# Kernel optimization log

Hardware: AMD Instinct MI355X
Metric: run time of the kernel (lower is better)

Reference implementation:

```python
import jax, jax.numpy as jnp
import numpy as np

D, P, S, E = 200, 200, 150, 150  # drugs, proteins, diseases, side-effects
EMB = 256

def setup_inputs() -> dict:
    key = jax.random.key(0)
    ks = jax.random.split(key, 10)
    s = 0.05
    type_mask = jnp.concatenate([
        jnp.zeros(D, jnp.int64) if False else jnp.full((D,), 0, jnp.int32),
        jnp.full((P,), 1, jnp.int32),
        jnp.full((S,), 2, jnp.int32),
        jnp.full((E,), 3, jnp.int32)]).astype(jnp.int32)
    return {
        'type_mask': type_mask,
        'entity_embedding': jax.random.normal(ks[0], (D + P + S + E, EMB)) * s,
        'relation_embedding': jax.random.normal(ks[1], (1200, EMB)) * s,
        'W_ent': jax.random.normal(ks[2], (EMB, EMB)) * s,
        'W_rel': jax.random.normal(ks[3], (EMB, EMB)) * s,
        'W1': jax.random.normal(ks[4], (2 * EMB, 1024)) * s,
        'b1': jnp.zeros((1024,)),
        'W2': jax.random.normal(ks[5], (1024, 512)) * s,
        'b2': jnp.zeros((512,)),
        'W3': jax.random.normal(ks[6], (512, 2)) * s,
        'b3': jnp.zeros((2,)),
    }

def _pair_softmax(a, b, W1, b1, W2, b2, W3, b3):
    # classifier(concat(a[i], b[j])) for the full cartesian product.
    # First linear is decomposed: W1 @ [a;b] = a@W1a + b@W1b (same math,
    # avoids materializing the [Na*Nb, 2*EMB] concat tensor).
    W1a, W1b = W1[:EMB], W1[EMB:]
    ha = a @ W1a                      # [Na, 1024]
    hb = b @ W1b                      # [Nb, 1024]
    h = jax.nn.relu(ha[:, None, :] + hb[None, :, :] + b1)  # [Na, Nb, 1024]
    h = jax.nn.relu(h @ W2 + b2)      # [Na, Nb, 512]
    logits = h @ W3 + b3              # [Na, Nb, 2]
    Na, Nb = a.shape[0], b.shape[0]
    return jax.nn.softmax(logits.reshape(Na * Nb, 2), axis=-1)

def reference(type_mask, entity_embedding, relation_embedding, W_ent, W_rel,
              W1, b1, W2, b2, W3, b3):
    tm = np.asarray(type_mask)  # concrete, block-structured type ids
    idx = [np.nonzero(tm == t)[0] for t in range(4)]
    # project embeddings (project_on path; nn.Linear: x @ W)
    ent = entity_embedding @ W_ent
    _rel = relation_embedding @ W_rel  # computed in original forward, unused (graph_on off)
    drug, prot, dis, se = (ent[idx[0]], ent[idx[1]], ent[idx[2]], ent[idx[3]])
    cls = lambda a, b: _pair_softmax(a, b, W1, b1, W2, b2, W3, b3)
    out_dp = cls(drug, prot)
    out_dd = cls(drug, drug)
    out_ds = cls(drug, dis)
    out_de = cls(drug, se)
    out_ps = cls(prot, dis)
    out_pp = cls(prot, prot)
    out_pd = cls(prot, drug)
    out_ed = cls(se, drug)
    out_sp = cls(dis, prot)
    out_sd = cls(dis, drug)
    return (out_dp, out_dd, out_ds, out_de, out_ps, out_pp, out_pd,
            out_ed, out_sp, out_sd, drug)
```

## Files before the change

kernel.cpp:

```cpp
#include <hip/hip_runtime.h>
#include <hip/hip_bf16.h>

typedef __attribute__((ext_vector_type(4))) float floatx4;
typedef __attribute__((ext_vector_type(8))) __bf16 bf16x8;
typedef unsigned short ushort_t;

#define NENT  700
#define EMB   256
#define KDIM  1024
#define NDIM  512
#define HROWS 720
#define NPAIR 340000

#define WS_HA   0
#define WS_HB   (WS_HA + HROWS*KDIM*2)
#define WS_W2H  (WS_HB + HROWS*KDIM*2)
#define WS_ENT  (WS_W2H + NDIM*KDIM*2)
#define WS_LG   (WS_ENT + NENT*EMB*4)

__device__ __forceinline__ float ldin(const void* p, int i, int isbf) {
    return isbf ? __bfloat162float(((const __hip_bfloat16*)p)[i])
                : ((const float*)p)[i];
}

__device__ __forceinline__ int detect_bf16(const ushort_t* __restrict__ w) {
    int t = threadIdx.x & 63;
    int e = (w[2*t] >> 7) & 0xFF;
    unsigned long long m = __ballot(e >= 100 && e <= 126);
    return (__popcll(m) >= 48) ? 1 : 0;
}

#define LDS_BARRIER() do { __builtin_amdgcn_s_waitcnt(0xC07F); __builtin_amdgcn_s_barrier(); } while (0)

__global__ void entprep_kernel(const void* __restrict__ E, const void* __restrict__ Went,
                               const void* __restrict__ W2,
                               float* __restrict__ ent, __hip_bfloat16* __restrict__ W2H,
                               void* __restrict__ out) {
    int isbf = detect_bf16((const ushort_t*)E);
    if (blockIdx.x < 88) {
        int ib = blockIdx.x * 8, t = threadIdx.x;
        __shared__ float rows[8][EMB];
#pragma unroll
        for (int r = 0; r < 8; ++r) {
            int i = ib + r;
            rows[r][t] = (i < NENT) ? ldin(E, i*EMB + t, isbf) : 0.f;
        }
        __syncthreads();
        float acc[8] = {0.f,0.f,0.f,0.f,0.f,0.f,0.f,0.f};
        if (isbf) {
            const __hip_bfloat16* W = (const __hip_bfloat16*)Went;
            for (int k = 0; k < EMB; ++k) {
                float w = __bfloat162float(W[k*EMB + t]);
#pragma unroll
                for (int r = 0; r < 8; ++r) acc[r] += rows[r][k] * w;
            }
        } else {
            const float* W = (const float*)Went;
            for (int k = 0; k < EMB; ++k) {
                float w = W[k*EMB + t];
#pragma unroll
                for (int r = 0; r < 8; ++r) acc[r] += rows[r][k] * w;
            }
        }
#pragma unroll
        for (int r = 0; r < 8; ++r) {
            int i = ib + r;
            if (i < NENT) {
                ent[i*EMB + t] = acc[r];
                if (i < 200) {
                    if (isbf) ((__hip_bfloat16*)out)[680000 + i*EMB + t] = __float2bfloat16(acc[r]);
                    else      ((float*)out)[680000 + i*EMB + t] = acc[r];
                }
            }
        }
    } else {
        int g = (blockIdx.x - 88)*256 + threadIdx.x;
        int lane = g & 63, f = (g >> 6) & 15, kc = (g >> 10) & 31, half = g >> 15;
        int l15 = lane & 15, quad = lane >> 4;
        int n = half*256 + f*16 + l15;
        bf16x8 v;
#pragma unroll
        for (int j = 0; j < 8; ++j) {
            int k = kc*32 + quad*8 + j;
            v[j] = (__bf16)ldin(W2, k*NDIM + n, isbf);
        }
        *(bf16x8*)(W2H + (size_t)g*8) = v;
    }
}

__global__ void hab_kernel(const float* __restrict__ ent, const void* __restrict__ E,
                           const void* __restrict__ W1, const void* __restrict__ b1,
                           __hip_bfloat16* __restrict__ HA, __hip_bfloat16* __restrict__ HB) {
    int isbf = detect_bf16((const ushort_t*)E);
    int part = blockIdx.y;
    int ib = blockIdx.x * 16;
    int t = threadIdx.x;
    __shared__ float rows[16][EMB];
#pragma unroll
    for (int r = 0; r < 16; ++r) {
        int i = ib + r;
        rows[r][t] = (i < NENT) ? ent[i*EMB + t] : 0.f;
    }
    __syncthreads();
    float acc[16][4];
#pragma unroll
    for (int r = 0; r < 16; ++r)
#pragma unroll
        for (int p = 0; p < 4; ++p) acc[r][p] = 0.f;

    int wbase = part*EMB*KDIM;
    if (isbf) {
        const __hip_bfloat16* W = (const __hip_bfloat16*)W1;
        for (int k = 0; k < EMB; ++k) {
            float w[4];
#pragma unroll
            for (int p = 0; p < 4; ++p) w[p] = __bfloat162float(W[wbase + k*KDIM + t + p*256]);
#pragma unroll
            for (int r = 0; r < 16; ++r) {
                float e = rows[r][k];
#pragma unroll
                for (int p = 0; p < 4; ++p) acc[r][p] += e * w[p];
            }
        }
    } else {
        const float* W = (const float*)W1;
        for (int k = 0; k < EMB; ++k) {
            float w[4];
#pragma unroll
            for (int p = 0; p < 4; ++p) w[p] = W[wbase + k*KDIM + t + p*256];
#pragma unroll
            for (int r = 0; r < 16; ++r) {
                float e = rows[r][k];
#pragma unroll
                for (int p = 0; p < 4; ++p) acc[r][p] += e * w[p];
            }
        }
    }
    __hip_bfloat16* HX = part ? HB : HA;
#pragma unroll
    for (int r = 0; r < 16; ++r) {
#pragma unroll
        for (int p = 0; p < 4; ++p) {
            int n = t + p*256;
            float v = acc[r][p];
            if (!part) v += ldin(b1, n, isbf);
            HX[(ib + r)*KDIM + n] = __float2bfloat16(v);
        }
    }
}

union U8 { bf16x8 v; unsigned u[4]; };

__device__ __forceinline__ bf16x8 mk_af3(bf16x8 ha, bf16x8 hb) {
    U8 r;
#pragma unroll
    for (int j = 0; j < 4; ++j) {
        float x0 = fmaxf((float)ha[2*j]   + (float)hb[2*j],   0.f);
        float x1 = fmaxf((float)ha[2*j+1] + (float)hb[2*j+1], 0.f);
        unsigned u0 = __float_as_uint(x0) + 0x8000u;
        unsigned u1 = __float_as_uint(x1) + 0x8000u;
#if defined(__has_builtin) && __has_builtin(__builtin_amdgcn_perm)
        r.u[j] = __builtin_amdgcn_perm(u1, u0, 0x07060302u);
#else
        r.u[j] = (u0 >> 16) | (u1 & 0xFFFF0000u);
#endif
    }
    return r.v;
}

#define MFMA(a, b, c) __builtin_amdgcn_mfma_f32_16x16x32_bf16((a), (b), (c), 0, 0, 0)

__global__ __launch_bounds__(512, 2) void pair_kernel(
        const ushort_t* __restrict__ HA, const ushort_t* __restrict__ HB,
        const ushort_t* __restrict__ W2H, const void* __restrict__ E,
        const void* __restrict__ b2, const void* __restrict__ W3,
        const void* __restrict__ b3, void* __restrict__ out) {

    const int blkEnd[10] = {325,650,900,1150,1400,1725,2050,2297,2544,2791};
    const int aB[10]  = {0,0,0,0,200,200,200,550,400,400};
    const int bB[10]  = {200,0,400,550,400,200,0,0,200,0};
    const int NaT[10] = {200,200,200,200,200,200,200,150,150,150};
    const int NbT[10] = {200,200,150,150,150,200,200,200,200,200};
    const int jTl[10] = {13,13,10,10,10,13,13,13,13,13};
    const int oOf[10] = {0,80000,160000,220000,280000,340000,420000,500000,560000,620000};

    __shared__ __align__(16) unsigned char sAF[32768];
    __shared__ float lgt[8][128][2];

    int bid = blockIdx.x;
    int ty = 0;
    while (bid >= blkEnd[ty]) ty++;
    int lb = bid - (ty ? blkEnd[ty-1] : 0);
    int jT = jTl[ty];
    int it = lb / jT;
    int jt = lb - it*jT;
    int i0 = aB[ty] + it*8;
    int j0 = bB[ty] + jt*16;

    int tid  = threadIdx.x;
    int lane = tid & 63;
    int w    = tid >> 6;
    int kcw  = w & 1;
    int mp   = (w >> 1) * 2;
    int l15  = lane & 15;
    int quad = lane >> 4;
    int kb   = (bid*7) & 31;

    const char* WB = (const char*)W2H + ((size_t)((w>>2)*512 + (w&3)*4))*1024 + lane*16;
    const ushort_t* HBp  = HB + (j0 + l15)*KDIM + quad*8;
    const ushort_t* HAp0 = HA + (i0 + mp)*KDIM + quad*8;
    const ushort_t* HAp1 = HAp0 + KDIM;

    floatx4 acc[8][4];
#pragma unroll
    for (int mf = 0; mf < 8; ++mf)
#pragma unroll
        for (int nf = 0; nf < 4; ++nf) acc[mf][nf] = (floatx4){0.f,0.f,0.f,0.f};

    int k0 = kb, k1 = (kb + 1) & 31;
    bf16x8 Bc0 = *(const bf16x8*)(WB + (size_t)k0*16384);
    bf16x8 Bc1 = *(const bf16x8*)(WB + (size_t)k0*16384 + 1024);
    bf16x8 Bc2 = *(const bf16x8*)(WB + (size_t)k0*16384 + 2048);
    bf16x8 Bc3 = *(const bf16x8*)(WB + (size_t)k0*16384 + 3072);
    bf16x8 Bn0 = *(const bf16x8*)(WB + (size_t)k1*16384);
    bf16x8 Bn1 = *(const bf16x8*)(WB + (size_t)k1*16384 + 1024);
    bf16x8 Bn2 = *(const bf16x8*)(WB + (size_t)k1*16384 + 2048);
    bf16x8 Bn3 = *(const bf16x8*)(WB + (size_t)k1*16384 + 3072);

    int kg0 = (kb + kcw) & 31;
    bf16x8 ha0 = *(const bf16x8*)(HAp0 + kg0*32);
    bf16x8 ha1 = *(const bf16x8*)(HAp1 + kg0*32);
    bf16x8 hb  = *(const bf16x8*)(HBp + kg0*32);

#define MFMA4(mf, x, B0, B1, B2, B3)                         \
    acc[mf][0] = MFMA(x, B0, acc[mf][0]);                    \
    acc[mf][1] = MFMA(x, B1, acc[mf][1]);                    \
    acc[mf][2] = MFMA(x, B2, acc[mf][2]);                    \
    acc[mf][3] = MFMA(x, B3, acc[mf][3]);

#pragma unroll 2
    for (int ph = 0; ph < 16; ++ph) {
        char* sW = (char*)sAF + (ph & 1)*16384 + kcw*8192 + mp*1024 + lane*16;
        *(bf16x8*)(sW)        = mk_af3(ha0, hb);
        *(bf16x8*)(sW + 1024) = mk_af3(ha1, hb);
        int kgn = (kb + 2*(ph + 1) + kcw) & 31;
        ha0 = *(const bf16x8*)(HAp0 + kgn*32);
        ha1 = *(const bf16x8*)(HAp1 + kgn*32);
        hb  = *(const bf16x8*)(HBp + kgn*32);
        LDS_BARRIER();

        const char* sR = (const char*)sAF + (ph & 1)*16384 + lane*16;
        int kn2 = (kb + 2*ph + 2) & 31;
        int kn3 = (kb + 2*ph + 3) & 31;
        {
            bf16x8 x0 = *(const bf16x8*)(sR);
            bf16x8 x1 = *(const bf16x8*)(sR + 1024);
            bf16x8 x2 = *(const bf16x8*)(sR + 2048);
            MFMA4(0, x0, Bc0, Bc1, Bc2, Bc3); x0 = *(const bf16x8*)(sR + 3072);
            MFMA4(1, x1, Bc0, Bc1, Bc2, Bc3); x1 = *(const bf16x8*)(sR + 4096);
            MFMA4(2, x2, Bc0, Bc1, Bc2, Bc3); x2 = *(const bf16x8*)(sR + 5120);
            MFMA4(3, x0, Bc0, Bc1, Bc2, Bc3); x0 = *(const bf16x8*)(sR + 6144);
            MFMA4(4, x1, Bc0, Bc1, Bc2, Bc3); x1 = *(const bf16x8*)(sR + 7168);
            MFMA4(5, x2, Bc0, Bc1, Bc2, Bc3);
            MFMA4(6, x0, Bc0, Bc1, Bc2, Bc3);
            MFMA4(7, x1, Bc0, Bc1, Bc2, Bc3);
        }
        Bc0 = *(const bf16x8*)(WB + (size_t)kn2*16384);
        Bc1 = *(const bf16x8*)(WB + (size_t)kn2*16384 + 1024);
        Bc2 = *(const bf16x8*)(WB + (size_t)kn2*16384 + 2048);
        Bc3 = *(const bf16x8*)(WB + (size_t)kn2*16384 + 3072);
        {
            bf16x8 x0 = *(const bf16x8*)(sR + 8192);
            bf16x8 x1 = *(const bf16x8*)(sR + 8192 + 1024);
            bf16x8 x2 = *(const bf16x8*)(sR + 8192 + 2048);
            MFMA4(0, x0, Bn0, Bn1, Bn2, Bn3); x0 = *(const bf16x8*)(sR + 8192 + 3072);
            MFMA4(1, x1, Bn0, Bn1, Bn2, Bn3); x1 = *(const bf16x8*)(sR + 8192 + 4096);
            MFMA4(2, x2, Bn0, Bn1, Bn2, Bn3); x2 = *(const bf16x8*)(sR + 8192 + 5120);
            MFMA4(3, x0, Bn0, Bn1, Bn2, Bn3); x0 = *(const bf16x8*)(sR + 8192 + 6144);
            MFMA4(4, x1, Bn0, Bn1, Bn2, Bn3); x1 = *(const bf16x8*)(sR + 8192 + 7168);
            MFMA4(5, x2, Bn0, Bn1, Bn2, Bn3);
            MFMA4(6, x0, Bn0, Bn1, Bn2, Bn3);
            MFMA4(7, x1, Bn0, Bn1, Bn2, Bn3);
        }
        Bn0 = *(const bf16x8*)(WB + (size_t)kn3*16384);
        Bn1 = *(const bf16x8*)(WB + (size_t)kn3*16384 + 1024);
        Bn2 = *(const bf16x8*)(WB + (size_t)kn3*16384 + 2048);
        Bn3 = *(const bf16x8*)(WB + (size_t)kn3*16384 + 3072);
    }
#undef MFMA4

    int isbf = detect_bf16((const ushort_t*)E);
    int nb = w*64;
    float b2v[4], wa[4], wb[4];
#pragma unroll
    for (int nf = 0; nf < 4; ++nf) {
        int n = nb + nf*16 + l15;
        b2v[nf] = ldin(b2, n, isbf);
        wa[nf]  = ldin(W3, 2*n, isbf);
        wb[nf]  = ldin(W3, 2*n+1, isbf);
    }
#pragma unroll
    for (int mf = 0; mf < 8; ++mf) {
        float s0[4] = {0.f,0.f,0.f,0.f};
        float s1[4] = {0.f,0.f,0.f,0.f};
#pragma unroll
        for (int nf = 0; nf < 4; ++nf) {
            floatx4 c = acc[mf][nf];
#pragma unroll
            for (int r = 0; r < 4; ++r) {
                float v = fmaxf(c[r] + b2v[nf], 0.f);
                s0[r] += v * wa[nf];
                s1[r] += v * wb[nf];
            }
        }
#pragma unroll
        for (int off = 1; off < 16; off <<= 1) {
#pragma unroll
            for (int r = 0; r < 4; ++r) {
                s0[r] += __shfl_xor(s0[r], off, 64);
                s1[r] += __shfl_xor(s1[r], off, 64);
            }
        }
        if (l15 == 0) {
#pragma unroll
            for (int r = 0; r < 4; ++r) {
                int p = mf*16 + quad*4 + r;
                lgt[w][p][0] = s0[r];
                lgt[w][p][1] = s1[r];
            }
        }
    }
    __syncthreads();

    if (tid < 128) {
        int p = tid;
        float l0 = 0.f, l1 = 0.f;
#pragma unroll
        for (int ww = 0; ww < 8; ++ww) { l0 += lgt[ww][p][0]; l1 += lgt[ww][p][1]; }
        l0 += ldin(b3, 0, isbf);
        l1 += ldin(b3, 1, isbf);
        int pi = it*8 + (p >> 4), pj = jt*16 + (p & 15);
        if (pi < NaT[ty] && pj < NbT[ty]) {
            float mx = fmaxf(l0, l1);
            float e0 = __expf(l0 - mx), e1 = __expf(l1 - mx);
            float inv = 1.f / (e0 + e1);
            int o = oOf[ty] + (pi*NbT[ty] + pj)*2;
            if (isbf) {
                __hip_bfloat16* ob = (__hip_bfloat16*)out;
                ob[o]   = __float2bfloat16(e0 * inv);
                ob[o+1] = __float2bfloat16(e1 * inv);
            } else {
                float* of = (float*)out;
                of[o]   = e0 * inv;
                of[o+1] = e1 * inv;
            }
        }
    }
}

extern "C" void kernel_launch(void* const* d_in, const int* in_sizes, int n_in,
                              void* d_out, int out_size, void* d_ws, size_t ws_size,
                              hipStream_t stream) {
    const void* E    = d_in[1];
    const void* Went = d_in[3];
    const void* W1   = d_in[5];
    const void* b1   = d_in[6];
    const void* W2   = d_in[7];
    const void* b2   = d_in[8];
    const void* W3   = d_in[9];
    const void* b3   = d_in[10];

    char* ws = (char*)d_ws;
    __hip_bfloat16* HA   = (__hip_bfloat16*)(ws + WS_HA);
    __hip_bfloat16* HB   = (__hip_bfloat16*)(ws + WS_HB);
    __hip_bfloat16* W2H  = (__hip_bfloat16*)(ws + WS_W2H);
    float*          entf = (float*)(ws + WS_ENT);

    entprep_kernel<<<dim3(344), dim3(256), 0, stream>>>(E, Went, W2, entf, W2H, d_out);
    hab_kernel<<<dim3(45, 2), dim3(256), 0, stream>>>(entf, E, W1, b1, HA, HB);
    pair_kernel<<<dim3(2791), dim3(512), 0, stream>>>((const ushort_t*)HA, (const ushort_t*)HB,
                                                      (const ushort_t*)W2H, E, b2, W3, b3, d_out);
}
```

Baseline: 514.8 us.

## Halve pair tile rows and give each wave both N halves of W2

The pair kernel now uses 256-thread blocks covering 4 A-rows by 16 B-columns (64 pairs) instead of 8x16, with twice as many blocks. Each of the 4 waves now covers 128 output columns (two 64-column slices from each N half), holding 8 B fragments and a 4x8 accumulator tile. The aim is better load balance and occupancy with smaller blocks and less LDS. In exchange, W2 fragments are reused across fewer pair rows per block, so more W2 traffic from L2, and the main loop is no longer unrolled.

```diff
diff --git a/kernel.cpp b/kernel.cpp
--- a/kernel.cpp
+++ b/kernel.cpp
@@ -170,13 +170,13 @@
 
 #define MFMA(a, b, c) __builtin_amdgcn_mfma_f32_16x16x32_bf16((a), (b), (c), 0, 0, 0)
 
-__global__ __launch_bounds__(512, 2) void pair_kernel(
+__global__ __launch_bounds__(256, 2) void pair_kernel(
         const ushort_t* __restrict__ HA, const ushort_t* __restrict__ HB,
         const ushort_t* __restrict__ W2H, const void* __restrict__ E,
         const void* __restrict__ b2, const void* __restrict__ W3,
         const void* __restrict__ b3, void* __restrict__ out) {
 
-    const int blkEnd[10] = {325,650,900,1150,1400,1725,2050,2297,2544,2791};
+    const int blkEnd[10] = {650,1300,1800,2300,2800,3450,4100,4594,5088,5582};
     const int aB[10]  = {0,0,0,0,200,200,200,550,400,400};
     const int bB[10]  = {200,0,400,550,400,200,0,0,200,0};
     const int NaT[10] = {200,200,200,200,200,200,200,150,150,150};
@@ -184,8 +184,8 @@
     const int jTl[10] = {13,13,10,10,10,13,13,13,13,13};
     const int oOf[10] = {0,80000,160000,220000,280000,340000,420000,500000,560000,620000};
 
-    __shared__ __align__(16) unsigned char sAF[32768];
-    __shared__ float lgt[8][128][2];
+    __shared__ __align__(16) unsigned char sAF[16384];
+    __shared__ float lgt[4][64][2];
 
     int bid = blockIdx.x;
     int ty = 0;
@@ -194,7 +194,7 @@
     int jT = jTl[ty];
     int it = lb / jT;
     int jt = lb - it*jT;
-    int i0 = aB[ty] + it*8;
+    int i0 = aB[ty] + it*4;
     int j0 = bB[ty] + jt*16;
 
     int tid  = threadIdx.x;
@@ -206,111 +206,93 @@
     int quad = lane >> 4;
     int kb   = (bid*7) & 31;
 
-    const char* WB = (const char*)W2H + ((size_t)((w>>2)*512 + (w&3)*4))*1024 + lane*16;
+    const char* WB0 = (const char*)W2H + (size_t)(w*4)*1024 + lane*16;
+    const char* WB1 = WB0 + (size_t)512*1024;
     const ushort_t* HBp  = HB + (j0 + l15)*KDIM + quad*8;
     const ushort_t* HAp0 = HA + (i0 + mp)*KDIM + quad*8;
     const ushort_t* HAp1 = HAp0 + KDIM;
 
-    floatx4 acc[8][4];
-#pragma unroll
-    for (int mf = 0; mf < 8; ++mf)
-#pragma unroll
-        for (int nf = 0; nf < 4; ++nf) acc[mf][nf] = (floatx4){0.f,0.f,0.f,0.f};
-
+    floatx4 acc[4][8];
+#pragma unroll
+    for (int mf = 0; mf < 4; ++mf)
+#pragma unroll
+        for (int hf = 0; hf < 8; ++hf) acc[mf][hf] = (floatx4){0.f,0.f,0.f,0.f};
+
+    bf16x8 Bc[2][4], Bn[2][4];
     int k0 = kb, k1 = (kb + 1) & 31;
-    bf16x8 Bc0 = *(const bf16x8*)(WB + (size_t)k0*16384);
-    bf16x8 Bc1 = *(const bf16x8*)(WB + (size_t)k0*16384 + 1024);
-    bf16x8 Bc2 = *(const bf16x8*)(WB + (size_t)k0*16384 + 2048);
-    bf16x8 Bc3 = *(const bf16x8*)(WB + (size_t)k0*16384 + 3072);
-    bf16x8 Bn0 = *(const bf16x8*)(WB + (size_t)k1*16384);
-    bf16x8 Bn1 = *(const bf16x8*)(WB + (size_t)k1*16384 + 1024);
-    bf16x8 Bn2 = *(const bf16x8*)(WB + (size_t)k1*16384 + 2048);
-    bf16x8 Bn3 = *(const bf16x8*)(WB + (size_t)k1*16384 + 3072);
-
+#pragma unroll
+    for (int nf = 0; nf < 4; ++nf) {
+        Bc[0][nf] = *(const bf16x8*)(WB0 + (size_t)k0*16384 + nf*1024);
+        Bc[1][nf] = *(const bf16x8*)(WB1 + (size_t)k0*16384 + nf*1024);
+        Bn[0][nf] = *(const bf16x8*)(WB0 + (size_t)k1*16384 + nf*1024);
+        Bn[1][nf] = *(const bf16x8*)(WB1 + (size_t)k1*16384 + nf*1024);
+    }
     int kg0 = (kb + kcw) & 31;
     bf16x8 ha0 = *(const bf16x8*)(HAp0 + kg0*32);
     bf16x8 ha1 = *(const bf16x8*)(HAp1 + kg0*32);
     bf16x8 hb  = *(const bf16x8*)(HBp + kg0*32);
 
-#define MFMA4(mf, x, B0, B1, B2, B3)                         \
-    acc[mf][0] = MFMA(x, B0, acc[mf][0]);                    \
-    acc[mf][1] = MFMA(x, B1, acc[mf][1]);                    \
-    acc[mf][2] = MFMA(x, B2, acc[mf][2]);                    \
-    acc[mf][3] = MFMA(x, B3, acc[mf][3]);
-
-#pragma unroll 2
+#pragma unroll 1
     for (int ph = 0; ph < 16; ++ph) {
-        char* sW = (char*)sAF + (ph & 1)*16384 + kcw*8192 + mp*1024 + lane*16;
+        char* sW = (char*)sAF + (ph & 1)*8192 + kcw*4096 + mp*1024 + lane*16;
         *(bf16x8*)(sW)        = mk_af3(ha0, hb);
         *(bf16x8*)(sW + 1024) = mk_af3(ha1, hb);
-        int kgn = (kb + 2*(ph + 1) + kcw) & 31;
+        int kgn = (kb + 2*ph + 2 + kcw) & 31;
         ha0 = *(const bf16x8*)(HAp0 + kgn*32);
         ha1 = *(const bf16x8*)(HAp1 + kgn*32);
         hb  = *(const bf16x8*)(HBp + kgn*32);
         LDS_BARRIER();
 
-        const char* sR = (const char*)sAF + (ph & 1)*16384 + lane*16;
+        const char* sR = (const char*)sAF + (ph & 1)*8192 + lane*16;
         int kn2 = (kb + 2*ph + 2) & 31;
         int kn3 = (kb + 2*ph + 3) & 31;
-        {
-            bf16x8 x0 = *(const bf16x8*)(sR);
-            bf16x8 x1 = *(const bf16x8*)(sR + 1024);
-            bf16x8 x2 = *(const bf16x8*)(sR + 2048);
-            MFMA4(0, x0, Bc0, Bc1, Bc2, Bc3); x0 = *(const bf16x8*)(sR + 3072);
-            MFMA4(1, x1, Bc0, Bc1, Bc2, Bc3); x1 = *(const bf16x8*)(sR + 4096);
-            MFMA4(2, x2, Bc0, Bc1, Bc2, Bc3); x2 = *(const bf16x8*)(sR + 5120);
-            MFMA4(3, x0, Bc0, Bc1, Bc2, Bc3); x0 = *(const bf16x8*)(sR + 6144);
-            MFMA4(4, x1, Bc0, Bc1, Bc2, Bc3); x1 = *(const bf16x8*)(sR + 7168);
-            MFMA4(5, x2, Bc0, Bc1, Bc2, Bc3);
-            MFMA4(6, x0, Bc0, Bc1, Bc2, Bc3);
-            MFMA4(7, x1, Bc0, Bc1, Bc2, Bc3);
-        }
-        Bc0 = *(const bf16x8*)(WB + (size_t)kn2*16384);
-        Bc1 = *(const bf16x8*)(WB + (size_t)kn2*16384 + 1024);
-        Bc2 = *(const bf16x8*)(WB + (size_t)kn2*16384 + 2048);
-        Bc3 = *(const bf16x8*)(WB + (size_t)kn2*16384 + 3072);
-        {
-            bf16x8 x0 = *(const bf16x8*)(sR + 8192);
-            bf16x8 x1 = *(const bf16x8*)(sR + 8192 + 1024);
-            bf16x8 x2 = *(const bf16x8*)(sR + 8192 + 2048);
-            MFMA4(0, x0, Bn0, Bn1, Bn2, Bn3); x0 = *(const bf16x8*)(sR + 8192 + 3072);
-            MFMA4(1, x1, Bn0, Bn1, Bn2, Bn3); x1 = *(const bf16x8*)(sR + 8192 + 4096);
-            MFMA4(2, x2, Bn0, Bn1, Bn2, Bn3); x2 = *(const bf16x8*)(sR + 8192 + 5120);
-            MFMA4(3, x0, Bn0, Bn1, Bn2, Bn3); x0 = *(const bf16x8*)(sR + 8192 + 6144);
-            MFMA4(4, x1, Bn0, Bn1, Bn2, Bn3); x1 = *(const bf16x8*)(sR + 8192 + 7168);
-            MFMA4(5, x2, Bn0, Bn1, Bn2, Bn3);
-            MFMA4(6, x0, Bn0, Bn1, Bn2, Bn3);
-            MFMA4(7, x1, Bn0, Bn1, Bn2, Bn3);
-        }
-        Bn0 = *(const bf16x8*)(WB + (size_t)kn3*16384);
-        Bn1 = *(const bf16x8*)(WB + (size_t)kn3*16384 + 1024);
-        Bn2 = *(const bf16x8*)(WB + (size_t)kn3*16384 + 2048);
-        Bn3 = *(const bf16x8*)(WB + (size_t)kn3*16384 + 3072);
-    }
-#undef MFMA4
+#pragma unroll
+        for (int m = 0; m < 4; ++m) {
+            bf16x8 a = *(const bf16x8*)(sR + m*1024);
+#pragma unroll
+            for (int hf = 0; hf < 8; ++hf)
+                acc[m][hf] = MFMA(a, Bc[hf>>2][hf&3], acc[m][hf]);
+        }
+#pragma unroll
+        for (int nf = 0; nf < 4; ++nf) {
+            Bc[0][nf] = *(const bf16x8*)(WB0 + (size_t)kn2*16384 + nf*1024);
+            Bc[1][nf] = *(const bf16x8*)(WB1 + (size_t)kn2*16384 + nf*1024);
+        }
+#pragma unroll
+        for (int m = 0; m < 4; ++m) {
+            bf16x8 a = *(const bf16x8*)(sR + 4096 + m*1024);
+#pragma unroll
+            for (int hf = 0; hf < 8; ++hf)
+                acc[m][hf] = MFMA(a, Bn[hf>>2][hf&3], acc[m][hf]);
+        }
+#pragma unroll
+        for (int nf = 0; nf < 4; ++nf) {
+            Bn[0][nf] = *(const bf16x8*)(WB0 + (size_t)kn3*16384 + nf*1024);
+            Bn[1][nf] = *(const bf16x8*)(WB1 + (size_t)kn3*16384 + nf*1024);
+        }
+    }
 
     int isbf = detect_bf16((const ushort_t*)E);
-    int nb = w*64;
-    float b2v[4], wa[4], wb[4];
-#pragma unroll
-    for (int nf = 0; nf < 4; ++nf) {
-        int n = nb + nf*16 + l15;
-        b2v[nf] = ldin(b2, n, isbf);
-        wa[nf]  = ldin(W3, 2*n, isbf);
-        wb[nf]  = ldin(W3, 2*n+1, isbf);
-    }
-#pragma unroll
-    for (int mf = 0; mf < 8; ++mf) {
+    float b2v[8], wa[8], wb[8];
+#pragma unroll
+    for (int hf = 0; hf < 8; ++hf) {
+        int n = (hf >> 2)*256 + w*64 + (hf & 3)*16 + l15;
+        b2v[hf] = ldin(b2, n, isbf);
+        wa[hf]  = ldin(W3, 2*n, isbf);
+        wb[hf]  = ldin(W3, 2*n+1, isbf);
+    }
+#pragma unroll
+    for (int mf = 0; mf < 4; ++mf) {
         float s0[4] = {0.f,0.f,0.f,0.f};
         float s1[4] = {0.f,0.f,0.f,0.f};
 #pragma unroll
-        for (int nf = 0; nf < 4; ++nf) {
-            floatx4 c = acc[mf][nf];
+        for (int hf = 0; hf < 8; ++hf) {
+            floatx4 c = acc[mf][hf];
 #pragma unroll
             for (int r = 0; r < 4; ++r) {
-                float v = fmaxf(c[r] + b2v[nf], 0.f);
-                s0[r] += v * wa[nf];
-                s1[r] += v * wb[nf];
+                float v = fmaxf(c[r] + b2v[hf], 0.f);
+                s0[r] += v * wa[hf];
+                s1[r] += v * wb[hf];
             }
         }
 #pragma unroll
@@ -332,14 +314,13 @@
     }
     __syncthreads();
 
-    if (tid < 128) {
+    if (tid < 64) {
         int p = tid;
-        float l0 = 0.f, l1 = 0.f;
-#pragma unroll
-        for (int ww = 0; ww < 8; ++ww) { l0 += lgt[ww][p][0]; l1 += lgt[ww][p][1]; }
+        float l0 = lgt[0][p][0] + lgt[1][p][0] + lgt[2][p][0] + lgt[3][p][0];
+        float l1 = lgt[0][p][1] + lgt[1][p][1] + lgt[2][p][1] + lgt[3][p][1];
         l0 += ldin(b3, 0, isbf);
         l1 += ldin(b3, 1, isbf);
-        int pi = it*8 + (p >> 4), pj = jt*16 + (p & 15);
+        int pi = it*4 + (p >> 4), pj = jt*16 + (p & 15);
         if (pi < NaT[ty] && pj < NbT[ty]) {
             float mx = fmaxf(l0, l1);
             float e0 = __expf(l0 - mx), e1 = __expf(l1 - mx);
@@ -378,6 +359,6 @@
 
     entprep_kernel<<<dim3(344), dim3(256), 0, stream>>>(E, Went, W2, entf, W2H, d_out);
     hab_kernel<<<dim3(45, 2), dim3(256), 0, stream>>>(entf, E, W1, b1, HA, HB);
-    pair_kernel<<<dim3(2791), dim3(512), 0, stream>>>((const ushort_t*)HA, (const ushort_t*)HB,
+    pair_kernel<<<dim3(5582), dim3(256), 0, stream>>>((const ushort_t*)HA, (const ushort_t*)HB,
                                                       (const ushort_t*)W2H, E, b2, W3, b3, d_out);
 }
```

Result: faster. 482.7 us (-6.2%).
